# Kernel optimization log

Hardware: AMD Instinct MI355X
Metric: run time of the kernel (lower is better)

The kernel has to match this reference:

```python
import jax, jax.numpy as jnp
import numpy as np

N, E, D = 524288, 50000, 64
COMMITMENT_COST = 0.25
EPS = 1e-6


def setup_inputs() -> dict:
    key = jax.random.key(0)
    k1, k2, k3 = jax.random.split(key, 3)
    inputs_all = jax.random.normal(k1, (N, D + 1), dtype=jnp.float32)
    # sorted unique genus taxids (even integers) -> codebook rows 0..E-1
    genus_taxids_key = (2 * jnp.arange(E)).astype(jnp.int32)
    taxids = jax.random.randint(k2, (N,), 0, 2 * E, dtype=jnp.int32)
    lineages_all = jnp.stack([jnp.full((N,), -1, jnp.int32), taxids], axis=1)
    # original inits embeddings to zeros; use small noise so the manifold map is non-degenerate
    embeddings = 0.01 * jax.random.normal(k3, (E, D), dtype=jnp.float32)
    return {"inputs_all": inputs_all, "lineages_all": lineages_all,
            "embeddings": embeddings, "genus_taxids_key": genus_taxids_key}


def convert_codebook_lorentz(w):
    # w: [*, D] -> hyperboloid points [*, D+1]
    x = 3.0 * jnp.tanh(w)
    # Lorentz_inner_product(v, v) with v = pad(x, (1,0)) is sum(x^2)
    n = jnp.sqrt(jnp.clip(jnp.sum(x * x, axis=-1, keepdims=True), EPS, None))
    n = jnp.clip(n, None, 10.0)
    v = jnp.concatenate([jnp.zeros_like(n), x], axis=-1)          # [*, D+1]
    mu0 = jnp.concatenate([jnp.ones_like(n), jnp.zeros_like(x)], axis=-1)
    return jnp.cosh(n) * mu0 + jnp.sinh(n) * v / n


def geodesic_distance(a, b):
    lip = jnp.sum(a[..., 1:] * b[..., 1:], axis=-1) - a[..., 0] * b[..., 0]
    return jnp.arccosh(jnp.clip(-lip, 1.0 + EPS, None))


def reference(inputs_all, lineages_all, embeddings, genus_taxids_key):
    taxids = lineages_all[:, 1]
    # GPU-resident replacement of the host dict lookup: keys are sorted
    idx = jnp.searchsorted(genus_taxids_key, taxids)
    idx = jnp.clip(idx, 0, genus_taxids_key.shape[0] - 1)
    mask = genus_taxids_key[idx] == taxids                        # [N] bool, torch.isin

    quantized = convert_codebook_lorentz(embeddings[idx])         # [N, D+1]
    e_latent = geodesic_distance(jax.lax.stop_gradient(quantized), inputs_all)
    q_latent = geodesic_distance(quantized, jax.lax.stop_gradient(inputs_all))
    c_loss = q_latent + COMMITMENT_COST * e_latent                # [N]

    n_valid = jnp.maximum(jnp.sum(mask.astype(jnp.float32)), 1.0)
    mean_loss = jnp.sum(jnp.where(mask, c_loss, 0.0)) / n_valid   # mean over valid rows

    quantized_st = inputs_all + jax.lax.stop_gradient(quantized - inputs_all)
    quantized_all = jnp.where(mask[:, None], quantized_st, inputs_all)
    return mean_loss, quantized_all
```

## Files before the change

### kernel.cpp

```cpp
#include <hip/hip_runtime.h>


#define NBLOCKS 2048
#define NTHREADS 256
#define WAVES_PER_BLOCK (NTHREADS / 64)
#define CHUNK 64

__device__ __forceinline__ float waveReduceSum(float v) {
#pragma unroll
    for (int m = 32; m >= 1; m >>= 1) v += __shfl_xor(v, m, 64);
    return v;
}

__device__ __forceinline__ float fast_tanh(float x) {
    x = fminf(fmaxf(x, -15.0f), 15.0f);
    float e2 = __expf(2.0f * x);
    return (e2 - 1.0f) * __builtin_amdgcn_rcpf(e2 + 1.0f);
}

__global__ __launch_bounds__(256) void vq_table_init(int* __restrict__ table, int ts) {
    int i = blockIdx.x * 256 + threadIdx.x;
    if (i < ts) table[i] = -1;
}

__global__ __launch_bounds__(256) void vq_table_fill(const int* __restrict__ key,
                                                     int* __restrict__ table,
                                                     int E, int ts) {
    int i = blockIdx.x * 256 + threadIdx.x;
    if (i < E) {
        int k = key[i];
        if ((unsigned)k < (unsigned)ts) table[k] = i;
    }
}

__global__ __launch_bounds__(256) void vq_codebook(const float* __restrict__ emb,
                                                   float* __restrict__ cb, int E) {
    const int lane = threadIdx.x & 63;
    const int wave = (blockIdx.x * NTHREADS + threadIdx.x) >> 6;
    if (wave >= E) return;
    const float w = emb[(size_t)wave * 64 + lane];
    const float x = 3.0f * fast_tanh(w);
    float n2 = waveReduceSum(x * x);
    n2 = fmaxf(n2, 1e-6f);
    float n = fminf(sqrtf(n2), 10.0f);
    const float e  = __expf(n);
    const float ei = __builtin_amdgcn_rcpf(e);
    const float c  = 0.5f * (e + ei);
    const float s  = 0.5f * (e - ei) * __builtin_amdgcn_rcpf(n);
    float* cbRow = cb + (size_t)wave * 65;
    cbRow[1 + lane] = s * x;
    if (lane == 0) cbRow[0] = c;
}

__global__ __launch_bounds__(NTHREADS) void vq_main(
    const float* __restrict__ inputs,
    const int*   __restrict__ lineages,
    const float* __restrict__ cb,
    const int*   __restrict__ table,
    float* __restrict__ out,
    float* __restrict__ partialLoss,
    float* __restrict__ partialCnt,
    int N, int ts)
{
    const int lane        = threadIdx.x & 63;
    const int waveInBlock = threadIdx.x >> 6;
    const int waveGlobal  = blockIdx.x * WAVES_PER_BLOCK + waveInBlock;
    const int totalWaves  = gridDim.x * WAVES_PER_BLOCK;
    const int nChunks     = (N + CHUNK - 1) / CHUNK;

    float lossAcc = 0.0f, cntAcc = 0.0f;

    for (int chunk = waveGlobal; chunk < nChunks; chunk += totalWaves) {
        const int base = chunk * CHUNK;

        if (base + CHUNK <= N) {
            const int myRow   = base + lane;
            const int   t_l   = lineages[2 * (size_t)myRow + 1];
            const float in0_l = inputs[(size_t)myRow * 65];
            const int   idx_l = ((unsigned)t_l < (unsigned)ts) ? table[t_l] : -1;
            float c_l = in0_l;

#pragma unroll 8
            for (int j = 0; j < CHUNK; ++j) {
                const int   sidx    = __builtin_amdgcn_readlane(idx_l, j);
                const float in0     = __uint_as_float(
                    __builtin_amdgcn_readlane(__float_as_uint(in0_l), j));
                const bool  matched = sidx >= 0;

                const float* cbRow = cb + (size_t)(matched ? sidx : 0) * 65;
                const float cc = cbRow[0];
                const float qd = cbRow[1 + lane];
                const float* inRow = inputs + (size_t)(base + j) * 65;
                const float ind = inRow[1 + lane];

                const float dot = waveReduceSum(qd * ind);
                const float lip = dot - cc * in0;
                const float z   = fmaxf(-lip, 1.0f + 1e-6f);
                const float dist = __logf(z + sqrtf(fmaxf(z * z - 1.0f, 0.0f)));
                lossAcc += matched ? 1.25f * dist : 0.0f;
                cntAcc  += matched ? 1.0f : 0.0f;

                out[1 + (size_t)(base + j) * 65 + 1 + lane] = matched ? qd : ind;
                const float tc = matched ? cc : in0;
                c_l = (lane == j) ? tc : c_l;
            }
            out[1 + (size_t)myRow * 65] = c_l;
        } else {
            for (int j = 0; j < CHUNK; ++j) {
                const int row = base + j;
                if (row >= N) break;
                const int t = lineages[2 * (size_t)row + 1];
                const int idx = ((unsigned)t < (unsigned)ts) ? table[t] : -1;
                const float* inRow = inputs + (size_t)row * 65;
                const float in0 = inRow[0];
                const float ind = inRow[1 + lane];
                float* outRow = out + 1 + (size_t)row * 65;
                if (idx >= 0) {
                    const float* cbRow = cb + (size_t)idx * 65;
                    const float cc = cbRow[0];
                    const float qd = cbRow[1 + lane];
                    const float dot = waveReduceSum(qd * ind);
                    const float z = fmaxf(-(dot - cc * in0), 1.0f + 1e-6f);
                    const float dist = __logf(z + sqrtf(fmaxf(z * z - 1.0f, 0.0f)));
                    if (lane == 0) { lossAcc += 1.25f * dist; cntAcc += 1.0f; }
                    lossAcc = __shfl(lossAcc, 0, 64);
                    cntAcc  = __shfl(cntAcc, 0, 64);
                    outRow[1 + lane] = qd;
                    if (lane == 0) outRow[0] = cc;
                } else {
                    outRow[1 + lane] = ind;
                    if (lane == 0) outRow[0] = in0;
                }
            }
        }
    }

    __shared__ float sLoss[WAVES_PER_BLOCK];
    __shared__ float sCnt[WAVES_PER_BLOCK];
    if (lane == 0) { sLoss[waveInBlock] = lossAcc; sCnt[waveInBlock] = cntAcc; }
    __syncthreads();
    if (threadIdx.x == 0) {
        float L = 0.0f, C = 0.0f;
#pragma unroll
        for (int i = 0; i < WAVES_PER_BLOCK; i++) { L += sLoss[i]; C += sCnt[i]; }
        partialLoss[blockIdx.x] = L;
        partialCnt[blockIdx.x]  = C;
    }
}

__global__ __launch_bounds__(256) void vq_finalize(
    const float* __restrict__ partialLoss,
    const float* __restrict__ partialCnt,
    float* __restrict__ out, int nParts)
{
    __shared__ float sL[256];
    __shared__ float sC[256];
    float L = 0.0f, C = 0.0f;
    for (int i = threadIdx.x; i < nParts; i += 256) {
        L += partialLoss[i];
        C += partialCnt[i];
    }
    sL[threadIdx.x] = L; sC[threadIdx.x] = C;
    __syncthreads();
    if (threadIdx.x == 0) {
        float tl = 0.0f, tc = 0.0f;
        for (int i = 0; i < 256; i++) { tl += sL[i]; tc += sC[i]; }
        out[0] = tl / fmaxf(tc, 1.0f);
    }
}

extern "C" void kernel_launch(void* const* d_in, const int* in_sizes, int n_in,
                              void* d_out, int out_size, void* d_ws, size_t ws_size,
                              hipStream_t stream) {
    const float* inputs   = (const float*)d_in[0];
    const int*   lineages = (const int*)d_in[1];
    const float* emb      = (const float*)d_in[2];
    const int*   key      = (const int*)d_in[3];
    const int E = in_sizes[3];
    const int N = in_sizes[0] / 65;
    const int ts = 2 * E;

    float* out = (float*)d_out;
    char*  ws  = (char*)d_ws;
    int*   table = (int*)ws;
    float* cb    = (float*)(ws + (size_t)ts * sizeof(int));
    float* partialLoss = cb + (size_t)E * 65;
    float* partialCnt  = partialLoss + NBLOCKS;

    vq_table_init<<<(ts + 255) / 256, 256, 0, stream>>>(table, ts);
    vq_table_fill<<<(E + 255) / 256, 256, 0, stream>>>(key, table, E, ts);
    vq_codebook<<<(E * 64 + NTHREADS - 1) / NTHREADS, NTHREADS, 0, stream>>>(emb, cb, E);
    vq_main<<<NBLOCKS, NTHREADS, 0, stream>>>(inputs, lineages, cb, table,
                                              out, partialLoss, partialCnt, N, ts);
    vq_finalize<<<1, 256, 0, stream>>>(partialLoss, partialCnt, out, NBLOCKS);
}
```

Measured before the change: 319.4 us.

## Skip unmatched-row work, split wave reductions via LDS, use nontemporal accesses

In the full-chunk path, each row now branches on whether it matched. Unmatched rows skip the codebook load and the dot-product reduction and just copy the input. For matched rows, the 64-lane reduction is cut to four xor-shuffle steps, and the 16-lane partial sums go into per-wave shared memory. Each lane then finishes the dot product, the arccosh distance and the first-column output for its own row after the loop, so the scalar tail math runs once per lane instead of redundantly per row. Input/output streams use nontemporal loads and stores, and loss accumulators are reduced across the wave only at the end. Costs are extra LDS traffic and a divergent-free but branchy inner loop.

```diff
diff --git a/kernel.cpp b/kernel.cpp
--- a/kernel.cpp
+++ b/kernel.cpp
@@ -68,6 +68,9 @@
     const int totalWaves  = gridDim.x * WAVES_PER_BLOCK;
     const int nChunks     = (N + CHUNK - 1) / CHUNK;
 
+    __shared__ float T[WAVES_PER_BLOCK][CHUNK * 5];
+    float* Tw = T[waveInBlock];
+
     float lossAcc = 0.0f, cntAcc = 0.0f;
 
     for (int chunk = waveGlobal; chunk < nChunks; chunk += totalWaves) {
@@ -75,36 +78,43 @@
 
         if (base + CHUNK <= N) {
             const int myRow   = base + lane;
-            const int   t_l   = lineages[2 * (size_t)myRow + 1];
-            const float in0_l = inputs[(size_t)myRow * 65];
+            const int   t_l   = __builtin_nontemporal_load(&lineages[2 * (size_t)myRow + 1]);
+            const float in0_l = __builtin_nontemporal_load(&inputs[(size_t)myRow * 65]);
             const int   idx_l = ((unsigned)t_l < (unsigned)ts) ? table[t_l] : -1;
-            float c_l = in0_l;
+            const bool  matched_l = idx_l >= 0;
 
 #pragma unroll 8
             for (int j = 0; j < CHUNK; ++j) {
-                const int   sidx    = __builtin_amdgcn_readlane(idx_l, j);
-                const float in0     = __uint_as_float(
-                    __builtin_amdgcn_readlane(__float_as_uint(in0_l), j));
-                const bool  matched = sidx >= 0;
-
-                const float* cbRow = cb + (size_t)(matched ? sidx : 0) * 65;
-                const float cc = cbRow[0];
-                const float qd = cbRow[1 + lane];
+                const int sidx = __builtin_amdgcn_readlane(idx_l, j);
                 const float* inRow = inputs + (size_t)(base + j) * 65;
-                const float ind = inRow[1 + lane];
-
-                const float dot = waveReduceSum(qd * ind);
-                const float lip = dot - cc * in0;
-                const float z   = fmaxf(-lip, 1.0f + 1e-6f);
-                const float dist = __logf(z + sqrtf(fmaxf(z * z - 1.0f, 0.0f)));
-                lossAcc += matched ? 1.25f * dist : 0.0f;
-                cntAcc  += matched ? 1.0f : 0.0f;
-
-                out[1 + (size_t)(base + j) * 65 + 1 + lane] = matched ? qd : ind;
-                const float tc = matched ? cc : in0;
-                c_l = (lane == j) ? tc : c_l;
+                const float ind = __builtin_nontemporal_load(&inRow[1 + lane]);
+                float* oRow = out + 1 + (size_t)(base + j) * 65;
+
+                if (sidx >= 0) {
+                    const float qd = cb[(size_t)sidx * 65 + 1 + lane];
+                    float p = qd * ind;
+                    p += __shfl_xor(p, 1, 64);
+                    p += __shfl_xor(p, 2, 64);
+                    p += __shfl_xor(p, 4, 64);
+                    p += __shfl_xor(p, 8, 64);
+                    if ((lane & 15) == 0) Tw[j * 5 + (lane >> 4)] = p;
+                    __builtin_nontemporal_store(qd, &oRow[1 + lane]);
+                } else {
+                    __builtin_nontemporal_store(ind, &oRow[1 + lane]);
+                }
             }
-            out[1 + (size_t)myRow * 65] = c_l;
+
+            const float dot = Tw[lane * 5 + 0] + Tw[lane * 5 + 1]
+                            + Tw[lane * 5 + 2] + Tw[lane * 5 + 3];
+            const int   cidx = matched_l ? idx_l : 0;
+            const float cc   = cb[(size_t)cidx * 65];
+            const float tc   = matched_l ? cc : in0_l;
+            const float lip  = dot - cc * in0_l;
+            const float z    = fmaxf(-lip, 1.0f + 1e-6f);
+            const float dist = __logf(z + sqrtf(fmaxf(z * z - 1.0f, 0.0f)));
+            lossAcc += matched_l ? 1.25f * dist : 0.0f;
+            cntAcc  += matched_l ? 1.0f : 0.0f;
+            __builtin_nontemporal_store(tc, &out[1 + (size_t)myRow * 65]);
         } else {
             for (int j = 0; j < CHUNK; ++j) {
                 const int row = base + j;
@@ -123,8 +133,6 @@
                     const float z = fmaxf(-(dot - cc * in0), 1.0f + 1e-6f);
                     const float dist = __logf(z + sqrtf(fmaxf(z * z - 1.0f, 0.0f)));
                     if (lane == 0) { lossAcc += 1.25f * dist; cntAcc += 1.0f; }
-                    lossAcc = __shfl(lossAcc, 0, 64);
-                    cntAcc  = __shfl(cntAcc, 0, 64);
                     outRow[1 + lane] = qd;
                     if (lane == 0) outRow[0] = cc;
                 } else {
@@ -135,6 +143,8 @@
         }
     }
 
+    lossAcc = waveReduceSum(lossAcc);
+    cntAcc  = waveReduceSum(cntAcc);
     __shared__ float sLoss[WAVES_PER_BLOCK];
     __shared__ float sCnt[WAVES_PER_BLOCK];
     if (lane == 0) { sLoss[waveInBlock] = lossAcc; sCnt[waveInBlock] = cntAcc; }
```

Measured after the change: 353.1 us. +10.6%, slower.
